# Kernel optimization log

Measured on AMD Instinct MI355X. Metric: run time of the kernel, lower is better.

Reference implementation:

```python
import jax, jax.numpy as jnp
import numpy as np
import math

EMB = 2048
NH = 16
HD = EMB // NH
T = 4096
EPS = 1e-5


def setup_inputs() -> dict:
    key = jax.random.key(0)
    ks = jax.random.split(key, 8)
    lim = 1.0 / math.sqrt(EMB)
    q = jax.random.normal(ks[0], (T, EMB), dtype=jnp.float32)
    k = jax.random.normal(ks[1], (T, EMB), dtype=jnp.float32)
    v = jax.random.normal(ks[2], (T, EMB), dtype=jnp.float32)
    Wq = jax.random.uniform(ks[3], (EMB, EMB), minval=-lim, maxval=lim, dtype=jnp.float32)
    Wk = jax.random.uniform(ks[4], (EMB, EMB), minval=-lim, maxval=lim, dtype=jnp.float32)
    Wv = jax.random.uniform(ks[5], (EMB, EMB), minval=-lim, maxval=lim, dtype=jnp.float32)
    Wo = jax.random.uniform(ks[6], (EMB, EMB), minval=-lim, maxval=lim, dtype=jnp.float32)
    ln_w = jnp.ones((EMB,), dtype=jnp.float32)
    mask = jnp.tril(jnp.ones((T, T), dtype=jnp.int32))  # causal
    return {"q": q, "k": k, "v": v, "Wq": Wq, "Wk": Wk, "Wv": Wv,
            "Wo": Wo, "ln_w": ln_w, "mask": mask}


def reference(q, k, v, Wq, Wk, Wv, Wo, ln_w, mask):
    scale = 1.0 / math.sqrt(HD)
    # projections (Linear is weight @ x, i.e. x @ W^T)
    Q = (q @ Wq.T).reshape(T, NH, HD).transpose(1, 0, 2)   # [nh, T, hd]
    K = (k @ Wk.T).reshape(T, NH, HD).transpose(1, 0, 2)
    V = (v @ Wv.T).reshape(T, NH, HD).transpose(1, 0, 2)
    A = jnp.einsum('htd,hsd->hts', Q, K) * scale           # [nh, T, T]
    A = jnp.where(mask != 0, A, -jnp.inf)
    P = jax.nn.softmax(A, axis=-1)
    y = jnp.einsum('hts,hsd->htd', P, V)                   # [nh, T, hd]
    y = y.transpose(1, 0, 2).reshape(T, EMB)               # concat heads
    y = y @ Wo.T
    # deterministic dropout = identity; add residue; per-token LayerNorm (scale only)
    x = y + q
    mu = jnp.mean(x, axis=-1, keepdims=True)
    var = jnp.var(x, axis=-1, keepdims=True)
    return (x - mu) * jax.lax.rsqrt(var + EPS) * ln_w
```

## Files before the change

### kernel.cpp

```cpp
#include <hip/hip_runtime.h>

typedef __bf16 bf16x8 __attribute__((ext_vector_type(8)));
typedef __bf16 bf16x2_t __attribute__((ext_vector_type(2)));
typedef float f32x4 __attribute__((ext_vector_type(4)));
typedef float f32x16 __attribute__((ext_vector_type(16)));
typedef unsigned int u32x4 __attribute__((ext_vector_type(4)));

#define EMB 2048
#define NH 16
#define HD 128
#define TSEQ 4096

__device__ __forceinline__ unsigned short f2bf(float x) {
  unsigned int u = __builtin_bit_cast(unsigned int, x);
  u += 0x7fffu + ((u >> 16) & 1u);
  return (unsigned short)(u >> 16);
}

__device__ __forceinline__ void gl_lds16(const void* g, void* l) {
  __builtin_amdgcn_global_load_lds((__attribute__((address_space(1))) void*)(void*)g,
                                   (__attribute__((address_space(3))) void*)l, 16, 0, 0);
}

template <typename OutT>
__device__ __forceinline__ void store_out(OutT* p, float v) {
  if constexpr (sizeof(OutT) == 2) { *p = f2bf(v); } else { *p = v; }
}

__global__ __launch_bounds__(256) void cvt_all(const float* __restrict__ q, const float* __restrict__ k,
                                               const float* __restrict__ v, const float* __restrict__ Wq,
                                               const float* __restrict__ Wk, const float* __restrict__ Wv,
                                               const float* __restrict__ Wo,
                                               unsigned short* qb, unsigned short* kb, unsigned short* vb,
                                               unsigned short* Wqb, unsigned short* Wkb, unsigned short* Wvb,
                                               unsigned short* Wob) {
  const int SX = TSEQ * EMB / 8;
  const int SW = EMB * EMB / 8;
  int i = blockIdx.x * 256 + threadIdx.x;
  const float* src; unsigned short* dst; int off;
  if (i < 3 * SX) {
    int seg = i >> 20; off = i & (SX - 1);
    src = (seg == 0) ? q : (seg == 1) ? k : v;
    dst = (seg == 0) ? qb : (seg == 1) ? kb : vb;
  } else {
    int j = i - 3 * SX;
    int seg = j >> 19; off = j & (SW - 1);
    src = (seg == 0) ? Wq : (seg == 1) ? Wk : (seg == 2) ? Wv : Wo;
    dst = (seg == 0) ? Wqb : (seg == 1) ? Wkb : (seg == 2) ? Wvb : Wob;
  }
  const float4* p = (const float4*)src + (size_t)off * 2;
  float4 a = p[0], b = p[1];
  u32x4 r;
  r.x = (unsigned)f2bf(a.x) | ((unsigned)f2bf(a.y) << 16);
  r.y = (unsigned)f2bf(a.z) | ((unsigned)f2bf(a.w) << 16);
  r.z = (unsigned)f2bf(b.x) | ((unsigned)f2bf(b.y) << 16);
  r.w = (unsigned)f2bf(b.z) | ((unsigned)f2bf(b.w) << 16);
  ((u32x4*)dst)[off] = r;
}

template <typename OutT>
__device__ __forceinline__ void gemm_body(const unsigned short* __restrict__ A,
                                          const unsigned short* __restrict__ B,
                                          OutT* __restrict__ C,
                                          int m0, int n0, int N, int K, char* smem) {
  char* sA = smem;
  char* sB = smem + 8192;
  const int t = threadIdx.x;
  const int l = t & 63, lg = l >> 4, l15 = l & 15;
  const int w = t >> 6, wm = w >> 1, wn = w & 1;

  f32x4 acc[4][4] = {};

  const int rowS = t >> 2;
  const int cbS = (t & 3) * 16;
  const char* Ab = (const char*)A + ((size_t)(m0 + rowS) * K) * 2 + cbS;
  const char* Bb = (const char*)B + ((size_t)(n0 + rowS) * K) * 2 + cbS;
  const size_t rowStep = (size_t)64 * K * 2;

  for (int kt = 0; kt < K; kt += 32) {
    __syncthreads();
    gl_lds16(Ab, sA + t * 16);
    gl_lds16(Ab + rowStep, sA + 4096 + t * 16);
    gl_lds16(Bb, sB + t * 16);
    gl_lds16(Bb + rowStep, sB + 4096 + t * 16);
    Ab += 64; Bb += 64;
    __syncthreads();

    bf16x8 af[4], bfr[4];
#pragma unroll
    for (int m = 0; m < 4; m++)
      af[m] = *(const bf16x8*)(sA + (wm * 64 + m * 16 + l15) * 64 + lg * 16);
#pragma unroll
    for (int n = 0; n < 4; n++)
      bfr[n] = *(const bf16x8*)(sB + (wn * 64 + n * 16 + l15) * 64 + lg * 16);
#pragma unroll
    for (int m = 0; m < 4; m++)
#pragma unroll
      for (int n = 0; n < 4; n++)
        acc[m][n] = __builtin_amdgcn_mfma_f32_16x16x32_bf16(af[m], bfr[n], acc[m][n], 0, 0, 0);
  }

#pragma unroll
  for (int m = 0; m < 4; m++) {
    int row = m0 + wm * 64 + m * 16 + 4 * lg;
#pragma unroll
    for (int n = 0; n < 4; n++) {
      int col = n0 + wn * 64 + n * 16 + l15;
#pragma unroll
      for (int i = 0; i < 4; i++)
        store_out(C + (size_t)(row + i) * N + col, acc[m][n][i]);
    }
  }
}

__global__ __launch_bounds__(256) void gemm_qkv(const unsigned short* __restrict__ qb,
                                                const unsigned short* __restrict__ kb,
                                                const unsigned short* __restrict__ vb,
                                                const unsigned short* __restrict__ Wq,
                                                const unsigned short* __restrict__ Wk,
                                                const unsigned short* __restrict__ Wv,
                                                unsigned short* Qo, unsigned short* Ko, unsigned short* Vto) {
  __shared__ char smem[16384];
  const int bx = blockIdx.x;
  const int z = bx >> 9, r = bx & 511;
  const unsigned short* A; const unsigned short* B; unsigned short* C;
  int N, m0, n0;
  if (z == 0)      { A = qb; B = Wq; C = Qo;  N = EMB;  n0 = (r & 15) << 7; m0 = (r >> 4) << 7; }
  else if (z == 1) { A = kb; B = Wk; C = Ko;  N = EMB;  n0 = (r & 15) << 7; m0 = (r >> 4) << 7; }
  else             { A = Wv; B = vb; C = Vto; N = TSEQ; n0 = (r & 31) << 7; m0 = (r >> 5) << 7; }
  gemm_body<unsigned short>(A, B, C, m0, n0, N, EMB, smem);
}

__global__ __launch_bounds__(256) void gemm_o(const unsigned short* __restrict__ A,
                                              const unsigned short* __restrict__ B,
                                              float* __restrict__ C) {
  __shared__ char smem[16384];
  gemm_body<float>(A, B, C, blockIdx.y * 128, blockIdx.x * 128, EMB, EMB, smem);
}

__global__ __launch_bounds__(256, 2) void attn_kernel(const unsigned short* __restrict__ Q,
                                                      const unsigned short* __restrict__ Kp,
                                                      const unsigned short* __restrict__ Vt,
                                                      unsigned short* __restrict__ Y) {
  __shared__ char sK[2][16384];
  __shared__ char sV[2][16384];
  const int t = threadIdx.x, l = t & 63, w = t >> 6;
  const int l31 = l & 31, hh = l >> 5;
  const int b = blockIdx.x;
  const int h = b >> 5;
  const int x = b & 31;
  const int tile = (h < 8) ? x : 31 - x;
  const int q0 = tile * 128;
  const int nIter = 2 * tile + 2;
  const int qrow = q0 + w * 32 + l31;

  bf16x8 qf[8];
#pragma unroll
  for (int kd = 0; kd < 8; kd++)
    qf[kd] = *(const bf16x8*)(Q + (size_t)qrow * EMB + h * HD + kd * 16 + hh * 8);

  f32x16 o[4] = {};
  float m_run = -1e30f, l_run = 0.0f;

  const int rK = t >> 4, cK = (t & 15) * 16;
  const int rV = t >> 3, cV = (t & 7) * 16;
  const char* Kb = (const char*)Kp;
  const char* Vb = (const char*)Vt;
  const float SC = 0.08838834764831845f;

  auto stage = [&](int buf, int kv0) {
#pragma unroll
    for (int c = 0; c < 4; c++) {
      int rowK = c * 16 + rK;
      gl_lds16(Kb + (size_t)(kv0 + rowK) * (EMB * 2) + h * (HD * 2) + (cK ^ ((rowK & 7) << 4)),
               sK[buf] + c * 4096 + t * 16);
      int rowV = c * 32 + rV;
      gl_lds16(Vb + (size_t)(h * HD + rowV) * (TSEQ * 2) + kv0 * 2 + (cV ^ ((rowV & 7) << 4)),
               sV[buf] + c * 4096 + t * 16);
    }
  };

  stage(0, 0);
  int cur = 0;
  for (int it = 0; it < nIter; ++it) {
    const int kv0 = it * 64;
    if (it + 1 < nIter) {
      stage(cur ^ 1, kv0 + 64);
      asm volatile("s_waitcnt vmcnt(8)" ::: "memory");
    } else {
      asm volatile("s_waitcnt vmcnt(0)" ::: "memory");
    }
    __builtin_amdgcn_s_barrier();

    const char* KB = sK[cur];
    const char* VB = sV[cur];

    f32x16 s[2] = {};
    __builtin_amdgcn_s_setprio(1);
#pragma unroll
    for (int kvm = 0; kvm < 2; kvm++) {
      const int rowA = kvm * 32 + l31;
      const int swz = (rowA & 7) << 4;
#pragma unroll
      for (int kd = 0; kd < 8; kd++) {
        bf16x8 kf = *(const bf16x8*)(KB + rowA * 256 + ((kd * 32 + hh * 16) ^ swz));
        s[kvm] = __builtin_amdgcn_mfma_f32_32x32x16_bf16(kf, qf[kd], s[kvm], 0, 0, 0);
      }
    }
    __builtin_amdgcn_s_setprio(0);

    const bool diag = (kv0 + 64 > q0);
    float bmax = -1e30f;
#pragma unroll
    for (int kvm = 0; kvm < 2; kvm++)
#pragma unroll
      for (int i = 0; i < 16; i++) {
        float xv = s[kvm][i] * SC;
        if (diag && (kv0 + kvm * 32 + (i & 3) + 8 * (i >> 2) + 4 * hh > qrow)) xv = -1e30f;
        s[kvm][i] = xv;
        bmax = fmaxf(bmax, xv);
      }
    bmax = fmaxf(bmax, __shfl_xor(bmax, 32, 64));
    const float m_new = fmaxf(m_run, bmax);
    const float resc = __expf(m_run - m_new);
    float psum = 0.0f;
    unsigned int wb[16];
#pragma unroll
    for (int kvm = 0; kvm < 2; kvm++)
#pragma unroll
      for (int m = 0; m < 8; m++) {
        float p0 = __expf(s[kvm][2 * m + 0] - m_new);
        float p1 = __expf(s[kvm][2 * m + 1] - m_new);
        psum += p0 + p1;
        bf16x2_t pk; pk[0] = (__bf16)p0; pk[1] = (__bf16)p1;
        wb[kvm * 8 + m] = __builtin_bit_cast(unsigned int, pk);
      }
    psum += __shfl_xor(psum, 32, 64);
    l_run = l_run * resc + psum;
    m_run = m_new;
#pragma unroll
    for (int hdm = 0; hdm < 4; hdm++)
#pragma unroll
      for (int i = 0; i < 16; i++) o[hdm][i] *= resc;

    __builtin_amdgcn_s_setprio(1);
#pragma unroll
    for (int kvm = 0; kvm < 2; kvm++)
#pragma unroll
      for (int sx = 0; sx < 2; sx++) {
        const int base = kvm * 8 + 4 * sx;
        const unsigned int a0 = wb[base + 0], a1 = wb[base + 1];
        const unsigned int b0 = wb[base + 2], b1 = wb[base + 3];
        const unsigned int snd0 = hh ? a0 : b0;
        const unsigned int snd1 = hh ? a1 : b1;
        const unsigned int rcv0 = (unsigned int)__shfl_xor((int)snd0, 32, 64);
        const unsigned int rcv1 = (unsigned int)__shfl_xor((int)snd1, 32, 64);
        u32x4 pw;
        pw.x = hh ? rcv0 : a0;
        pw.y = hh ? rcv1 : a1;
        pw.z = hh ? b0 : rcv0;
        pw.w = hh ? b1 : rcv1;
        const bf16x8 pfrag = __builtin_bit_cast(bf16x8, pw);
        const int ks = kvm * 2 + sx;
#pragma unroll
        for (int hdm = 0; hdm < 4; hdm++) {
          const int rowA = hdm * 32 + l31;
          bf16x8 vf = *(const bf16x8*)(VB + rowA * 128 + ((ks * 32 + hh * 16) ^ ((rowA & 7) << 4)));
          o[hdm] = __builtin_amdgcn_mfma_f32_32x32x16_bf16(vf, pfrag, o[hdm], 0, 0, 0);
        }
      }
    __builtin_amdgcn_s_setprio(0);
    __builtin_amdgcn_s_barrier();
    cur ^= 1;
  }

  const float inv = 1.0f / l_run;
#pragma unroll
  for (int hdm = 0; hdm < 4; hdm++)
#pragma unroll
    for (int rq = 0; rq < 4; rq++) {
      ushort4 st;
      st.x = f2bf(o[hdm][4 * rq + 0] * inv);
      st.y = f2bf(o[hdm][4 * rq + 1] * inv);
      st.z = f2bf(o[hdm][4 * rq + 2] * inv);
      st.w = f2bf(o[hdm][4 * rq + 3] * inv);
      *(ushort4*)(Y + (size_t)qrow * EMB + h * HD + hdm * 32 + 8 * rq + 4 * hh) = st;
    }
}

__global__ __launch_bounds__(256) void ln_kernel(const float* __restrict__ y2,
                                                 const float* __restrict__ qin,
                                                 const float* __restrict__ lnw,
                                                 float* __restrict__ out) {
  const int row = blockIdx.x, t = threadIdx.x;
  const float4* Y = (const float4*)(y2 + (size_t)row * EMB);
  const float4* Qv = (const float4*)(qin + (size_t)row * EMB);
  float4 a = Y[t], b = Qv[t];
  float4 x0, x1;
  x0.x = a.x + b.x; x0.y = a.y + b.y; x0.z = a.z + b.z; x0.w = a.w + b.w;
  a = Y[t + 256]; b = Qv[t + 256];
  x1.x = a.x + b.x; x1.y = a.y + b.y; x1.z = a.z + b.z; x1.w = a.w + b.w;
  float s = x0.x + x0.y + x0.z + x0.w + x1.x + x1.y + x1.z + x1.w;
  float s2 = x0.x * x0.x + x0.y * x0.y + x0.z * x0.z + x0.w * x0.w +
             x1.x * x1.x + x1.y * x1.y + x1.z * x1.z + x1.w * x1.w;
#pragma unroll
  for (int d = 1; d < 64; d <<= 1) {
    s += __shfl_xor(s, d, 64);
    s2 += __shfl_xor(s2, d, 64);
  }
  __shared__ float red[8];
  if ((t & 63) == 0) { red[(t >> 6) * 2] = s; red[(t >> 6) * 2 + 1] = s2; }
  __syncthreads();
  s = red[0] + red[2] + red[4] + red[6];
  s2 = red[1] + red[3] + red[5] + red[7];
  float mu = s * (1.0f / EMB);
  float var = s2 * (1.0f / EMB) - mu * mu;
  float r = rsqrtf(var + 1e-5f);
  float4 w0 = ((const float4*)lnw)[t], w1 = ((const float4*)lnw)[t + 256];
  float4 o0, o1;
  o0.x = (x0.x - mu) * r * w0.x; o0.y = (x0.y - mu) * r * w0.y;
  o0.z = (x0.z - mu) * r * w0.z; o0.w = (x0.w - mu) * r * w0.w;
  o1.x = (x1.x - mu) * r * w1.x; o1.y = (x1.y - mu) * r * w1.y;
  o1.z = (x1.z - mu) * r * w1.z; o1.w = (x1.w - mu) * r * w1.w;
  ((float4*)(out + (size_t)row * EMB))[t] = o0;
  ((float4*)(out + (size_t)row * EMB))[t + 256] = o1;
}

extern "C" void kernel_launch(void* const* d_in, const int* in_sizes, int n_in,
                              void* d_out, int out_size, void* d_ws, size_t ws_size,
                              hipStream_t stream) {
  const float* q = (const float*)d_in[0];
  const float* k = (const float*)d_in[1];
  const float* v = (const float*)d_in[2];
  const float* Wq = (const float*)d_in[3];
  const float* Wk = (const float*)d_in[4];
  const float* Wv = (const float*)d_in[5];
  const float* Wo = (const float*)d_in[6];
  const float* lnw = (const float*)d_in[7];
  float* out = (float*)d_out;
  char* ws = (char*)d_ws;

  const size_t WB = (size_t)EMB * EMB * 2;
  const size_t XB = (size_t)TSEQ * EMB * 2;
  unsigned short* Wq_b = (unsigned short*)(ws + 0 * WB);
  unsigned short* Wk_b = (unsigned short*)(ws + 1 * WB);
  unsigned short* Wv_b = (unsigned short*)(ws + 2 * WB);
  unsigned short* Wo_b = (unsigned short*)(ws + 3 * WB);
  unsigned short* qb   = (unsigned short*)(ws + 4 * WB);
  unsigned short* kb   = (unsigned short*)(ws + 4 * WB + XB);
  unsigned short* vb   = (unsigned short*)(ws + 4 * WB + 2 * XB);
  unsigned short* Qb   = (unsigned short*)(ws + 4 * WB + 3 * XB);
  unsigned short* Kb   = (unsigned short*)(ws + 4 * WB + 4 * XB);
  unsigned short* Vtb  = (unsigned short*)(ws + 4 * WB + 5 * XB);
  unsigned short* yb   = qb;
  float* y2 = (float*)(ws + 4 * WB + XB);

  cvt_all<<<20480, 256, 0, stream>>>(q, k, v, Wq, Wk, Wv, Wo,
                                     qb, kb, vb, Wq_b, Wk_b, Wv_b, Wo_b);

  gemm_qkv<<<1536, 256, 0, stream>>>(qb, kb, vb, Wq_b, Wk_b, Wv_b, Qb, Kb, Vtb);

  attn_kernel<<<512, 256, 0, stream>>>(Qb, Kb, Vtb, yb);

  gemm_o<<<dim3(16, 32), 256, 0, stream>>>(yb, Wo_b, y2);

  ln_kernel<<<TSEQ, 256, 0, stream>>>(y2, q, lnw, out);
}
```

Baseline: 378.0 us.

## Fold softmax scale into Q projection, use exp2 with lazy rescale, triple-buffer V

The softmax scale times log2(e) is folded into the Q projection epilogue so attention can use raw exp2 with no per-element multiply. Online-softmax rescaling of the output accumulator is skipped when the block max grows by at most 8 (in log2 units), which avoids vector multiplies on most iterations. V gets a third LDS buffer so the end-of-iteration barrier can move to right after QK^T. The K swizzle is widened to 16 rows to reduce bank conflicts. The extra LDS lowers occupancy headroom, and the lazy rescale lets exponents reach 2^8 before renormalising.

```diff
diff --git a/kernel.cpp b/kernel.cpp
--- a/kernel.cpp
+++ b/kernel.cpp
@@ -16,6 +16,8 @@
   u += 0x7fffu + ((u >> 16) & 1u);
   return (unsigned short)(u >> 16);
 }
+
+__device__ __forceinline__ float ex2(float x) { return __builtin_amdgcn_exp2f(x); }
 
 __device__ __forceinline__ void gl_lds16(const void* g, void* l) {
   __builtin_amdgcn_global_load_lds((__attribute__((address_space(1))) void*)(void*)g,
@@ -62,7 +64,7 @@
 __device__ __forceinline__ void gemm_body(const unsigned short* __restrict__ A,
                                           const unsigned short* __restrict__ B,
                                           OutT* __restrict__ C,
-                                          int m0, int n0, int N, int K, char* smem) {
+                                          int m0, int n0, int N, int K, char* smem, float oscale) {
   char* sA = smem;
   char* sB = smem + 8192;
   const int t = threadIdx.x;
@@ -108,7 +110,7 @@
       int col = n0 + wn * 64 + n * 16 + l15;
 #pragma unroll
       for (int i = 0; i < 4; i++)
-        store_out(C + (size_t)(row + i) * N + col, acc[m][n][i]);
+        store_out(C + (size_t)(row + i) * N + col, acc[m][n][i] * oscale);
     }
   }
 }
@@ -124,18 +126,18 @@
   const int bx = blockIdx.x;
   const int z = bx >> 9, r = bx & 511;
   const unsigned short* A; const unsigned short* B; unsigned short* C;
-  int N, m0, n0;
-  if (z == 0)      { A = qb; B = Wq; C = Qo;  N = EMB;  n0 = (r & 15) << 7; m0 = (r >> 4) << 7; }
-  else if (z == 1) { A = kb; B = Wk; C = Ko;  N = EMB;  n0 = (r & 15) << 7; m0 = (r >> 4) << 7; }
-  else             { A = Wv; B = vb; C = Vto; N = TSEQ; n0 = (r & 31) << 7; m0 = (r >> 5) << 7; }
-  gemm_body<unsigned short>(A, B, C, m0, n0, N, EMB, smem);
+  int N, m0, n0; float sc;
+  if (z == 0)      { A = qb; B = Wq; C = Qo;  N = EMB;  n0 = (r & 15) << 7; m0 = (r >> 4) << 7; sc = 0.12751743f; }
+  else if (z == 1) { A = kb; B = Wk; C = Ko;  N = EMB;  n0 = (r & 15) << 7; m0 = (r >> 4) << 7; sc = 1.0f; }
+  else             { A = Wv; B = vb; C = Vto; N = TSEQ; n0 = (r & 31) << 7; m0 = (r >> 5) << 7; sc = 1.0f; }
+  gemm_body<unsigned short>(A, B, C, m0, n0, N, EMB, smem, sc);
 }
 
 __global__ __launch_bounds__(256) void gemm_o(const unsigned short* __restrict__ A,
                                               const unsigned short* __restrict__ B,
                                               float* __restrict__ C) {
   __shared__ char smem[16384];
-  gemm_body<float>(A, B, C, blockIdx.y * 128, blockIdx.x * 128, EMB, EMB, smem);
+  gemm_body<float>(A, B, C, blockIdx.y * 128, blockIdx.x * 128, EMB, EMB, smem, 1.0f);
 }
 
 __global__ __launch_bounds__(256, 2) void attn_kernel(const unsigned short* __restrict__ Q,
@@ -143,7 +145,7 @@
                                                       const unsigned short* __restrict__ Vt,
                                                       unsigned short* __restrict__ Y) {
   __shared__ char sK[2][16384];
-  __shared__ char sV[2][16384];
+  __shared__ char sV[3][16384];
   const int t = threadIdx.x, l = t & 63, w = t >> 6;
   const int l31 = l & 31, hh = l >> 5;
   const int b = blockIdx.x;
@@ -166,41 +168,40 @@
   const int rV = t >> 3, cV = (t & 7) * 16;
   const char* Kb = (const char*)Kp;
   const char* Vb = (const char*)Vt;
-  const float SC = 0.08838834764831845f;
-
-  auto stage = [&](int buf, int kv0) {
+
+  auto stage = [&](int kbuf, int vbuf, int kv0) {
 #pragma unroll
     for (int c = 0; c < 4; c++) {
       int rowK = c * 16 + rK;
-      gl_lds16(Kb + (size_t)(kv0 + rowK) * (EMB * 2) + h * (HD * 2) + (cK ^ ((rowK & 7) << 4)),
-               sK[buf] + c * 4096 + t * 16);
+      gl_lds16(Kb + (size_t)(kv0 + rowK) * (EMB * 2) + h * (HD * 2) + (cK ^ ((rowK & 15) << 4)),
+               sK[kbuf] + c * 4096 + t * 16);
       int rowV = c * 32 + rV;
       gl_lds16(Vb + (size_t)(h * HD + rowV) * (TSEQ * 2) + kv0 * 2 + (cV ^ ((rowV & 7) << 4)),
-               sV[buf] + c * 4096 + t * 16);
+               sV[vbuf] + c * 4096 + t * 16);
     }
   };
 
-  stage(0, 0);
-  int cur = 0;
+  stage(0, 0, 0);
+  int kc = 0, vc = 0, vn = 1;
   for (int it = 0; it < nIter; ++it) {
     const int kv0 = it * 64;
     if (it + 1 < nIter) {
-      stage(cur ^ 1, kv0 + 64);
+      stage(kc ^ 1, vn, kv0 + 64);
       asm volatile("s_waitcnt vmcnt(8)" ::: "memory");
     } else {
       asm volatile("s_waitcnt vmcnt(0)" ::: "memory");
     }
     __builtin_amdgcn_s_barrier();
 
-    const char* KB = sK[cur];
-    const char* VB = sV[cur];
+    const char* KB = sK[kc];
+    const char* VB = sV[vc];
 
     f32x16 s[2] = {};
     __builtin_amdgcn_s_setprio(1);
 #pragma unroll
     for (int kvm = 0; kvm < 2; kvm++) {
       const int rowA = kvm * 32 + l31;
-      const int swz = (rowA & 7) << 4;
+      const int swz = (rowA & 15) << 4;
 #pragma unroll
       for (int kd = 0; kd < 8; kd++) {
         bf16x8 kf = *(const bf16x8*)(KB + rowA * 256 + ((kd * 32 + hh * 16) ^ swz));
@@ -208,40 +209,49 @@
       }
     }
     __builtin_amdgcn_s_setprio(0);
+    __builtin_amdgcn_s_barrier();
 
     const bool diag = (kv0 + 64 > q0);
+    if (diag) {
+#pragma unroll
+      for (int kvm = 0; kvm < 2; kvm++)
+#pragma unroll
+        for (int i = 0; i < 16; i++)
+          if (kv0 + kvm * 32 + (i & 3) + 8 * (i >> 2) + 4 * hh > qrow) s[kvm][i] = -1e30f;
+    }
     float bmax = -1e30f;
 #pragma unroll
     for (int kvm = 0; kvm < 2; kvm++)
 #pragma unroll
-      for (int i = 0; i < 16; i++) {
-        float xv = s[kvm][i] * SC;
-        if (diag && (kv0 + kvm * 32 + (i & 3) + 8 * (i >> 2) + 4 * hh > qrow)) xv = -1e30f;
-        s[kvm][i] = xv;
-        bmax = fmaxf(bmax, xv);
-      }
+      for (int i = 0; i < 16; i++) bmax = fmaxf(bmax, s[kvm][i]);
     bmax = fmaxf(bmax, __shfl_xor(bmax, 32, 64));
-    const float m_new = fmaxf(m_run, bmax);
-    const float resc = __expf(m_run - m_new);
+
+    const bool skip = __all(bmax <= m_run + 8.0f);
+    const float m_eff = skip ? m_run : fmaxf(m_run, bmax);
+
     float psum = 0.0f;
     unsigned int wb[16];
 #pragma unroll
     for (int kvm = 0; kvm < 2; kvm++)
 #pragma unroll
       for (int m = 0; m < 8; m++) {
-        float p0 = __expf(s[kvm][2 * m + 0] - m_new);
-        float p1 = __expf(s[kvm][2 * m + 1] - m_new);
+        float p0 = ex2(s[kvm][2 * m + 0] - m_eff);
+        float p1 = ex2(s[kvm][2 * m + 1] - m_eff);
         psum += p0 + p1;
         bf16x2_t pk; pk[0] = (__bf16)p0; pk[1] = (__bf16)p1;
         wb[kvm * 8 + m] = __builtin_bit_cast(unsigned int, pk);
       }
     psum += __shfl_xor(psum, 32, 64);
-    l_run = l_run * resc + psum;
-    m_run = m_new;
-#pragma unroll
-    for (int hdm = 0; hdm < 4; hdm++)
-#pragma unroll
-      for (int i = 0; i < 16; i++) o[hdm][i] *= resc;
+    if (!skip) {
+      const float resc = ex2(m_run - m_eff);
+#pragma unroll
+      for (int hdm = 0; hdm < 4; hdm++)
+#pragma unroll
+        for (int i = 0; i < 16; i++) o[hdm][i] *= resc;
+      l_run *= resc;
+      m_run = m_eff;
+    }
+    l_run += psum;
 
     __builtin_amdgcn_s_setprio(1);
 #pragma unroll
@@ -270,8 +280,10 @@
         }
       }
     __builtin_amdgcn_s_setprio(0);
-    __builtin_amdgcn_s_barrier();
-    cur ^= 1;
+
+    kc ^= 1;
+    vc = vn;
+    vn = (vn == 2) ? 0 : vn + 1;
   }
 
   const float inv = 1.0f / l_run;
```

After: 352.6 us. 6.7% less time.
